# Performance work log

Hardware: AMD Instinct MI355X
Metric: run time of the kernel (lower is better)

## Reference

```python
import jax, jax.numpy as jnp
import numpy as np

B, S, D, A, E = 32, 2048, 512, 64, 64
EPS = 1e-5

def setup_inputs() -> dict:
    key = jax.random.key(0)
    ks = jax.random.split(key, 12)
    sc = 0.02
    return {
        "source_embedding": jax.random.normal(ks[0], (B, E), jnp.float32),
        "inputs": jax.random.normal(ks[1], (B, S, D), jnp.float32),
        "down_w_W": sc * jax.random.normal(ks[2], (E, A * D), jnp.float32),
        "down_w_b": jnp.zeros((A * D,), jnp.float32),
        "down_b_W": sc * jax.random.normal(ks[3], (E, A), jnp.float32),
        "down_b_b": jnp.zeros((A,), jnp.float32),
        "up_w_W": sc * jax.random.normal(ks[4], (E, D * A), jnp.float32),
        "up_w_b": jnp.zeros((D * A,), jnp.float32),
        "up_b_W": sc * jax.random.normal(ks[5], (E, D), jnp.float32),
        "up_b_b": jnp.zeros((D,), jnp.float32),
        "pre_w_W": sc * jax.random.normal(ks[6], (E, D), jnp.float32),
        "pre_w_b": jnp.ones((D,), jnp.float32),
        "pre_b_W": sc * jax.random.normal(ks[7], (E, D), jnp.float32),
        "pre_b_b": jnp.zeros((D,), jnp.float32),
        "post_w_W": sc * jax.random.normal(ks[8], (E, D), jnp.float32),
        "post_w_b": jnp.ones((D,), jnp.float32),
        "post_b_W": sc * jax.random.normal(ks[9], (E, D), jnp.float32),
        "post_b_b": jnp.zeros((D,), jnp.float32),
    }

def _cond_ln(x, w, b):
    # x: [B,S,D]; w,b: [B,D] -> per-sample affine layernorm over last dim
    mean = jnp.mean(x, axis=2, keepdims=True)
    var = jnp.mean((x - mean) ** 2, axis=2, keepdims=True) + EPS
    return (x - mean) / jnp.sqrt(var) * w[:, None, :] + b[:, None, :]

def reference(source_embedding, inputs,
              down_w_W, down_w_b, down_b_W, down_b_b,
              up_w_W, up_w_b, up_b_W, up_b_b,
              pre_w_W, pre_w_b, pre_b_W, pre_b_b,
              post_w_W, post_w_b, post_b_W, post_b_b):
    emb = source_embedding  # [B,E]
    # hypernet-generated per-sample adapter weights
    w_down = (emb @ down_w_W + down_w_b).reshape(B, A, D)  # [B,A,D]
    b_down = emb @ down_b_W + down_b_b                      # [B,A]
    w_up = (emb @ up_w_W + up_w_b).reshape(B, D, A)         # [B,D,A]
    b_up = emb @ up_b_W + up_b_b                            # [B,D]
    # conditional pre layernorm
    pre_w = emb @ pre_w_W + pre_w_b
    pre_b = emb @ pre_b_W + pre_b_b
    z = _cond_ln(inputs, pre_w, pre_b)
    # adapter: down-proj, relu, up-proj (matmul with weight.transpose(1,2))
    down = jnp.einsum('bsd,bad->bsa', z, w_down) + b_down[:, None, :]
    mid = jax.nn.relu(down)
    out = jnp.einsum('bsa,bda->bsd', mid, w_up) + b_up[:, None, :]
    # conditional post layernorm
    post_w = emb @ post_w_W + post_w_b
    post_b = emb @ post_b_W + post_b_b
    out = _cond_ln(out, post_w, post_b)
    return out + inputs
```

## Files before the change

### kernel.cpp

```cpp
#include <hip/hip_runtime.h>

#define NB 32
#define NS 2048
#define ND 512
#define NA 64
#define NE 64

typedef __bf16 bf16x8 __attribute__((ext_vector_type(8)));
typedef float f32x4 __attribute__((ext_vector_type(4)));

__device__ __forceinline__ unsigned short f2bf(float f) {
    union { float f; unsigned u; } v; v.f = f;
    unsigned r = (v.u + 0x7fffu + ((v.u >> 16) & 1u)) >> 16;
    return (unsigned short)r;
}
__device__ __forceinline__ unsigned pk(float a, float b) {
    return (unsigned)f2bf(a) | ((unsigned)f2bf(b) << 16);
}

__global__ __launch_bounds__(256) void hyper_vec(
    const float* __restrict__ emb,
    const float* __restrict__ pwW, const float* __restrict__ pwb,
    const float* __restrict__ pbW, const float* __restrict__ pbb,
    const float* __restrict__ powW, const float* __restrict__ powb,
    const float* __restrict__ pobW, const float* __restrict__ pobb,
    const float* __restrict__ ubW, const float* __restrict__ ubb,
    const float* __restrict__ dbW, const float* __restrict__ dbb,
    float* __restrict__ vecs) {
    int gid = blockIdx.x * 256 + threadIdx.x;
    if (gid >= NB * 2624) return;
    int b = gid / 2624;
    int r = gid - b * 2624;
    const float* W; const float* bias; int off, width;
    if (r < 2560) {
        int v = r >> 9; off = r & 511; width = 512;
        switch (v) {
            case 0:  W = pwW;  bias = pwb;  break;
            case 1:  W = pbW;  bias = pbb;  break;
            case 2:  W = powW; bias = powb; break;
            case 3:  W = pobW; bias = pobb; break;
            default: W = ubW;  bias = ubb;  break;
        }
    } else {
        off = r - 2560; width = 64; W = dbW; bias = dbb;
    }
    float acc = bias[off];
    const float* e = emb + b * 64;
#pragma unroll 8
    for (int k = 0; k < 64; ++k) acc = fmaf(e[k], W[k * width + off], acc);
    vecs[gid] = acc;
}

__global__ __launch_bounds__(256) void hyper_pack(
    const float* __restrict__ emb,
    const float* __restrict__ dwW, const float* __restrict__ dwb,
    const float* __restrict__ uwW, const float* __restrict__ uwb,
    const float* __restrict__ vecs,
    unsigned short* __restrict__ wdfrag, unsigned short* __restrict__ wufrag,
    float* __restrict__ cvec) {
    __shared__ float Wt[64][128];
    __shared__ float embs[NB * NE];
    const int tid = threadIdx.x;
    const int lane = tid & 63;
    const int bx = blockIdx.x;
    const int mat = bx >> 8;
    const int chunk = bx & 255;
    const int base = chunk * 128;
    const int colo = tid & 127;
    const int bh = tid >> 7;
    const float* W = mat ? uwW : dwW;
    const float* bias = mat ? uwb : dwb;

    for (int i = tid; i < NB * NE; i += 256) embs[i] = emb[i];
    for (int i = tid; i < 64 * 32; i += 256) {
        int k = i >> 5, c = (i & 31) << 2;
        *(float4*)&Wt[k][c] = *(const float4*)&W[(size_t)k * 32768 + base + c];
    }
    __syncthreads();

    const int col = base + colo;
    const float bv = bias[col];
    float acc[16];
#pragma unroll
    for (int b = 0; b < 16; ++b) acc[b] = bv;

    for (int k0 = 0; k0 < 64; k0 += 4) {
        float w0 = Wt[k0][colo], w1 = Wt[k0 + 1][colo];
        float w2 = Wt[k0 + 2][colo], w3 = Wt[k0 + 3][colo];
#pragma unroll
        for (int b = 0; b < 16; ++b) {
            float4 e = *(const float4*)&embs[(bh * 16 + b) * 64 + k0];
            acc[b] = fmaf(e.x, w0, acc[b]);
            acc[b] = fmaf(e.y, w1, acc[b]);
            acc[b] = fmaf(e.z, w2, acc[b]);
            acc[b] = fmaf(e.w, w3, acc[b]);
        }
    }

    if (mat == 0) {
        int a = col >> 9, d = col & 511;
        size_t idx0 = ((size_t)((a >> 4) * 16 + (d >> 5)) * 64 +
                       (((d & 31) >> 3) * 16 + (a & 15))) * 8 + (d & 7);
#pragma unroll
        for (int b = 0; b < 16; ++b) {
            int bg = bh * 16 + b;
            float raw = acc[b];
            float pw = vecs[bg * 2624 + d];
            float pb = vecs[bg * 2624 + 512 + d];
            float f = raw * pw;
            wdfrag[idx0 + (size_t)bg * 32768] = f2bf(f);
            float c2v = f, c1v = raw * pb;
#pragma unroll
            for (int m = 1; m <= 32; m <<= 1) {
                c2v += __shfl_xor(c2v, m);
                c1v += __shfl_xor(c1v, m);
            }
            if (lane == 0) {
                atomicAdd(&cvec[bg * 128 + 2 * a], c1v);
                atomicAdd(&cvec[bg * 128 + 2 * a + 1], c2v);
            }
        }
    } else {
        int d = col >> 6, a = col & 63;
        size_t idx0 = ((size_t)((d >> 4) * 2 + (a >> 5)) * 64 +
                       (((a & 31) >> 3) * 16 + (d & 15))) * 8 + (a & 7);
#pragma unroll
        for (int b = 0; b < 16; ++b)
            wufrag[idx0 + (size_t)(bh * 16 + b) * 32768] = f2bf(acc[b]);
    }
}

__global__ __launch_bounds__(256, 5) void fused_adapter(
    const float* __restrict__ inp,
    const unsigned short* __restrict__ wdfold,
    const unsigned short* __restrict__ wufrag,
    const float* __restrict__ vecs,
    const float* __restrict__ cvec,
    float* __restrict__ out) {
    __shared__ __align__(16) unsigned short z_lds[16][520];
    __shared__ __align__(16) unsigned short mid_lds[16][72];
    __shared__ __align__(16) float coeff[1536];
    __shared__ __align__(16) float preS[16][4], preQ[16][4];
    __shared__ __align__(16) float postS[16][4], postQ[16][4];

    const int tid = threadIdx.x;
    const int lane = tid & 63;
    const int wave = tid >> 6;
    const int lanelo = lane & 15;
    const int quad = lane >> 4;
    const int bx = blockIdx.x;
    const int b = bx >> 7;
    const int s0 = (bx & 127) * 16;

    const float* vb = vecs + b * 2624;
    for (int i = tid; i < 384; i += 256)
        ((float4*)coeff)[i] = ((const float4*)(vb + 1024))[i];

    const float* xp = inp + ((size_t)b * NS + s0 + lanelo) * ND + wave * 128 + quad * 8;
    float s = 0.f, q = 0.f;
#pragma unroll
    for (int kc2 = 0; kc2 < 4; ++kc2) {
        float4 x0 = *(const float4*)(xp + kc2 * 32);
        float4 x1 = *(const float4*)(xp + kc2 * 32 + 4);
        s += (x0.x + x0.y + x0.z + x0.w) + (x1.x + x1.y + x1.z + x1.w);
        q = fmaf(x0.x, x0.x, q); q = fmaf(x0.y, x0.y, q);
        q = fmaf(x0.z, x0.z, q); q = fmaf(x0.w, x0.w, q);
        q = fmaf(x1.x, x1.x, q); q = fmaf(x1.y, x1.y, q);
        q = fmaf(x1.z, x1.z, q); q = fmaf(x1.w, x1.w, q);
        uint4 au;
        au.x = pk(x0.x, x0.y); au.y = pk(x0.z, x0.w);
        au.z = pk(x1.x, x1.y); au.w = pk(x1.z, x1.w);
        *(uint4*)&z_lds[lanelo][wave * 128 + kc2 * 32 + quad * 8] = au;
    }
    s += __shfl_xor(s, 16); s += __shfl_xor(s, 32);
    q += __shfl_xor(q, 16); q += __shfl_xor(q, 32);
    if (lane < 16) { preS[lane][wave] = s; preQ[lane][wave] = q; }
    __syncthreads();

    float rs[4], mrs[4];
#pragma unroll
    for (int r = 0; r < 4; ++r) {
        int row = quad * 4 + r;
        float4 S = *(const float4*)preS[row];
        float4 Q = *(const float4*)preQ[row];
        float ss = (S.x + S.y) + (S.z + S.w);
        float qq = (Q.x + Q.y) + (Q.z + Q.w);
        float mean = ss * (1.0f / 512.0f);
        float var = qq * (1.0f / 512.0f) - mean * mean;
        float rstd = rsqrtf(var + 1e-5f);
        rs[r] = rstd;
        mrs[r] = mean * rstd;
    }

    const unsigned short* wd = wdfold + (size_t)b * 32768;
    f32x4 accd = (f32x4){0.f, 0.f, 0.f, 0.f};
#pragma unroll
    for (int kc = 0; kc < 16; ++kc) {
        uint4 au = *(const uint4*)&z_lds[lanelo][kc * 32 + quad * 8];
        uint4 bu = *(const uint4*)(wd + ((size_t)(wave * 16 + kc) * 64 + lane) * 8);
        accd = __builtin_amdgcn_mfma_f32_16x16x32_bf16(
            __builtin_bit_cast(bf16x8, au), __builtin_bit_cast(bf16x8, bu), accd, 0, 0, 0);
    }
    const int a_col = wave * 16 + lanelo;
    float2 cc = *(const float2*)(cvec + b * 128 + 2 * a_col);
    float c1 = cc.x + vb[2560 + a_col];
#pragma unroll
    for (int r = 0; r < 4; ++r) {
        float v = fmaf(rs[r], accd[r], fmaf(-mrs[r], cc.y, c1));
        mid_lds[quad * 4 + r][a_col] = f2bf(fmaxf(v, 0.0f));
    }
    __syncthreads();

    uint4 a0u = *(const uint4*)&mid_lds[lanelo][quad * 8];
    uint4 a1u = *(const uint4*)&mid_lds[lanelo][32 + quad * 8];
    bf16x8 af0 = __builtin_bit_cast(bf16x8, a0u);
    bf16x8 af1 = __builtin_bit_cast(bf16x8, a1u);
    const unsigned short* wu = wufrag + (size_t)b * 32768;
    f32x4 acc8[8];
    float sum[4] = {0.f, 0.f, 0.f, 0.f}, sq[4] = {0.f, 0.f, 0.f, 0.f};
#pragma unroll
    for (int nt8 = 0; nt8 < 8; ++nt8) {
        int nt = wave * 8 + nt8;
        uint4 b0 = *(const uint4*)(wu + ((size_t)(nt * 2 + 0) * 64 + lane) * 8);
        uint4 b1 = *(const uint4*)(wu + ((size_t)(nt * 2 + 1) * 64 + lane) * 8);
        f32x4 a4 = (f32x4){0.f, 0.f, 0.f, 0.f};
        a4 = __builtin_amdgcn_mfma_f32_16x16x32_bf16(af0, __builtin_bit_cast(bf16x8, b0), a4, 0, 0, 0);
        a4 = __builtin_amdgcn_mfma_f32_16x16x32_bf16(af1, __builtin_bit_cast(bf16x8, b1), a4, 0, 0, 0);
        float bu = coeff[1024 + nt * 16 + lanelo];
#pragma unroll
        for (int r = 0; r < 4; ++r) {
            float y = a4[r] + bu;
            a4[r] = y;
            sum[r] += y;
            sq[r] = fmaf(y, y, sq[r]);
        }
        acc8[nt8] = a4;
    }
#pragma unroll
    for (int r = 0; r < 4; ++r) {
#pragma unroll
        for (int m = 1; m <= 8; m <<= 1) {
            sum[r] += __shfl_xor(sum[r], m);
            sq[r] += __shfl_xor(sq[r], m);
        }
    }
    if (lanelo == 0) {
#pragma unroll
        for (int r = 0; r < 4; ++r) {
            postS[quad * 4 + r][wave] = sum[r];
            postQ[quad * 4 + r][wave] = sq[r];
        }
    }
    __syncthreads();

    float mean2[4], rstd2[4];
#pragma unroll
    for (int r = 0; r < 4; ++r) {
        int row = quad * 4 + r;
        float4 S = *(const float4*)postS[row];
        float4 Q = *(const float4*)postQ[row];
        float ss = (S.x + S.y) + (S.z + S.w);
        float qq = (Q.x + Q.y) + (Q.z + Q.w);
        mean2[r] = ss * (1.0f / 512.0f);
        float v2 = qq * (1.0f / 512.0f) - mean2[r] * mean2[r];
        rstd2[r] = rsqrtf(v2 + 1e-5f);
    }

    const size_t obase = ((size_t)b * NS + s0) * ND;
#pragma unroll
    for (int nt8 = 0; nt8 < 8; ++nt8) {
        int col = (wave * 8 + nt8) * 16 + lanelo;
        float pw = coeff[col];
        float pb = coeff[512 + col];
#pragma unroll
        for (int r = 0; r < 4; ++r) {
            size_t off = obase + (size_t)(quad * 4 + r) * ND + col;
            out[off] = fmaf((acc8[nt8][r] - mean2[r]) * rstd2[r], pw, pb) + inp[off];
        }
    }
}

extern "C" void kernel_launch(void* const* d_in, const int* in_sizes, int n_in,
                              void* d_out, int out_size, void* d_ws, size_t ws_size,
                              hipStream_t stream) {
    const float* emb  = (const float*)d_in[0];
    const float* inp  = (const float*)d_in[1];
    const float* dwW  = (const float*)d_in[2];
    const float* dwb  = (const float*)d_in[3];
    const float* dbW  = (const float*)d_in[4];
    const float* dbb  = (const float*)d_in[5];
    const float* uwW  = (const float*)d_in[6];
    const float* uwb  = (const float*)d_in[7];
    const float* ubW  = (const float*)d_in[8];
    const float* ubb  = (const float*)d_in[9];
    const float* pwW  = (const float*)d_in[10];
    const float* pwb  = (const float*)d_in[11];
    const float* pbW  = (const float*)d_in[12];
    const float* pbb  = (const float*)d_in[13];
    const float* powW = (const float*)d_in[14];
    const float* powb = (const float*)d_in[15];
    const float* pobW = (const float*)d_in[16];
    const float* pobb = (const float*)d_in[17];

    unsigned short* wdfrag = (unsigned short*)d_ws;
    unsigned short* wufrag = wdfrag + (size_t)NB * 32768;
    float* vecs = (float*)(wufrag + (size_t)NB * 32768);
    float* cvec = vecs + (size_t)NB * 2624;

    hyper_vec<<<(NB * 2624 + 255) / 256, 256, 0, stream>>>(
        emb, pwW, pwb, pbW, pbb, powW, powb, pobW, pobb, ubW, ubb, dbW, dbb, vecs);
    hipMemsetAsync(cvec, 0, (size_t)NB * 128 * sizeof(float), stream);
    hyper_pack<<<512, 256, 0, stream>>>(emb, dwW, dwb, uwW, uwb, vecs,
                                        wdfrag, wufrag, cvec);
    fused_adapter<<<NB * (NS / 16), 256, 0, stream>>>(
        inp, wdfrag, wufrag, vecs, cvec, (float*)d_out);
}
```

Baseline: 331.9 us.

## Split down-projection over K across waves with LDS partial-sum reduction

```diff
diff --git a/kernel.cpp b/kernel.cpp
--- a/kernel.cpp
+++ b/kernel.cpp
@@ -130,14 +130,14 @@
     }
 }
 
-__global__ __launch_bounds__(256, 5) void fused_adapter(
+__global__ __launch_bounds__(256, 4) void fused_adapter(
     const float* __restrict__ inp,
     const unsigned short* __restrict__ wdfold,
     const unsigned short* __restrict__ wufrag,
     const float* __restrict__ vecs,
     const float* __restrict__ cvec,
     float* __restrict__ out) {
-    __shared__ __align__(16) unsigned short z_lds[16][520];
+    __shared__ __align__(16) float p_lds[4][16][68];
     __shared__ __align__(16) unsigned short mid_lds[16][72];
     __shared__ __align__(16) float coeff[1536];
     __shared__ __align__(16) float preS[16][4], preQ[16][4];
@@ -148,39 +148,66 @@
     const int wave = tid >> 6;
     const int lanelo = lane & 15;
     const int quad = lane >> 4;
-    const int bx = blockIdx.x;
+    const int bx0 = blockIdx.x;
+    const int bx = (bx0 & 7) * 512 + (bx0 >> 3);
     const int b = bx >> 7;
     const int s0 = (bx & 127) * 16;
 
     const float* vb = vecs + b * 2624;
+
+    const float* xp = inp + ((size_t)b * NS + s0 + lanelo) * ND + wave * 128 + quad * 8;
+    float4 x0[4], x1[4];
+#pragma unroll
+    for (int kc2 = 0; kc2 < 4; ++kc2) {
+        x0[kc2] = *(const float4*)(xp + kc2 * 32);
+        x1[kc2] = *(const float4*)(xp + kc2 * 32 + 4);
+    }
+
     for (int i = tid; i < 384; i += 256)
         ((float4*)coeff)[i] = ((const float4*)(vb + 1024))[i];
 
-    const float* xp = inp + ((size_t)b * NS + s0 + lanelo) * ND + wave * 128 + quad * 8;
+    uint4 au[4];
     float s = 0.f, q = 0.f;
 #pragma unroll
     for (int kc2 = 0; kc2 < 4; ++kc2) {
-        float4 x0 = *(const float4*)(xp + kc2 * 32);
-        float4 x1 = *(const float4*)(xp + kc2 * 32 + 4);
-        s += (x0.x + x0.y + x0.z + x0.w) + (x1.x + x1.y + x1.z + x1.w);
-        q = fmaf(x0.x, x0.x, q); q = fmaf(x0.y, x0.y, q);
-        q = fmaf(x0.z, x0.z, q); q = fmaf(x0.w, x0.w, q);
-        q = fmaf(x1.x, x1.x, q); q = fmaf(x1.y, x1.y, q);
-        q = fmaf(x1.z, x1.z, q); q = fmaf(x1.w, x1.w, q);
-        uint4 au;
-        au.x = pk(x0.x, x0.y); au.y = pk(x0.z, x0.w);
-        au.z = pk(x1.x, x1.y); au.w = pk(x1.z, x1.w);
-        *(uint4*)&z_lds[lanelo][wave * 128 + kc2 * 32 + quad * 8] = au;
+        float4 a = x0[kc2], c = x1[kc2];
+        s += (a.x + a.y + a.z + a.w) + (c.x + c.y + c.z + c.w);
+        q = fmaf(a.x, a.x, q); q = fmaf(a.y, a.y, q);
+        q = fmaf(a.z, a.z, q); q = fmaf(a.w, a.w, q);
+        q = fmaf(c.x, c.x, q); q = fmaf(c.y, c.y, q);
+        q = fmaf(c.z, c.z, q); q = fmaf(c.w, c.w, q);
+        au[kc2].x = pk(a.x, a.y); au[kc2].y = pk(a.z, a.w);
+        au[kc2].z = pk(c.x, c.y); au[kc2].w = pk(c.z, c.w);
     }
     s += __shfl_xor(s, 16); s += __shfl_xor(s, 32);
     q += __shfl_xor(q, 16); q += __shfl_xor(q, 32);
     if (lane < 16) { preS[lane][wave] = s; preQ[lane][wave] = q; }
+
+    const unsigned short* wd = wdfold + (size_t)b * 32768;
+    const unsigned short* wdp = wd + ((size_t)(wave * 4) * 64 + lane) * 8;
+    f32x4 acc[4];
+#pragma unroll
+    for (int nt = 0; nt < 4; ++nt) acc[nt] = (f32x4){0.f, 0.f, 0.f, 0.f};
+#pragma unroll
+    for (int kc2 = 0; kc2 < 4; ++kc2) {
+        bf16x8 af = __builtin_bit_cast(bf16x8, au[kc2]);
+#pragma unroll
+        for (int nt = 0; nt < 4; ++nt) {
+            uint4 bu = *(const uint4*)(wdp + (size_t)(nt * 16 + kc2) * 512);
+            acc[nt] = __builtin_amdgcn_mfma_f32_16x16x32_bf16(
+                af, __builtin_bit_cast(bf16x8, bu), acc[nt], 0, 0, 0);
+        }
+    }
+#pragma unroll
+    for (int nt = 0; nt < 4; ++nt)
+#pragma unroll
+        for (int r = 0; r < 4; ++r)
+            p_lds[wave][quad * 4 + r][nt * 16 + lanelo] = acc[nt][r];
     __syncthreads();
 
-    float rs[4], mrs[4];
-#pragma unroll
-    for (int r = 0; r < 4; ++r) {
-        int row = quad * 4 + r;
+    {
+        const int row = tid >> 4;
+        const int a0 = (tid & 15) << 2;
         float4 S = *(const float4*)preS[row];
         float4 Q = *(const float4*)preQ[row];
         float ss = (S.x + S.y) + (S.z + S.w);
@@ -188,26 +215,20 @@
         float mean = ss * (1.0f / 512.0f);
         float var = qq * (1.0f / 512.0f) - mean * mean;
         float rstd = rsqrtf(var + 1e-5f);
-        rs[r] = rstd;
-        mrs[r] = mean * rstd;
-    }
-
-    const unsigned short* wd = wdfold + (size_t)b * 32768;
-    f32x4 accd = (f32x4){0.f, 0.f, 0.f, 0.f};
-#pragma unroll
-    for (int kc = 0; kc < 16; ++kc) {
-        uint4 au = *(const uint4*)&z_lds[lanelo][kc * 32 + quad * 8];
-        uint4 bu = *(const uint4*)(wd + ((size_t)(wave * 16 + kc) * 64 + lane) * 8);
-        accd = __builtin_amdgcn_mfma_f32_16x16x32_bf16(
-            __builtin_bit_cast(bf16x8, au), __builtin_bit_cast(bf16x8, bu), accd, 0, 0, 0);
-    }
-    const int a_col = wave * 16 + lanelo;
-    float2 cc = *(const float2*)(cvec + b * 128 + 2 * a_col);
-    float c1 = cc.x + vb[2560 + a_col];
-#pragma unroll
-    for (int r = 0; r < 4; ++r) {
-        float v = fmaf(rs[r], accd[r], fmaf(-mrs[r], cc.y, c1));
-        mid_lds[quad * 4 + r][a_col] = f2bf(fmaxf(v, 0.0f));
+        float mrs = mean * rstd;
+        f32x4 v = *(const f32x4*)&p_lds[0][row][a0];
+        v = v + *(const f32x4*)&p_lds[1][row][a0];
+        v = v + *(const f32x4*)&p_lds[2][row][a0];
+        v = v + *(const f32x4*)&p_lds[3][row][a0];
+        float4 cv0 = *(const float4*)&cvec[b * 128 + 2 * a0];
+        float4 cv1 = *(const float4*)&cvec[b * 128 + 2 * a0 + 4];
+        float4 bd = *(const float4*)&vb[2560 + a0];
+        ushort4 m;
+        m.x = f2bf(fmaxf(fmaf(rstd, v[0], fmaf(-mrs, cv0.y, cv0.x + bd.x)), 0.f));
+        m.y = f2bf(fmaxf(fmaf(rstd, v[1], fmaf(-mrs, cv0.w, cv0.z + bd.y)), 0.f));
+        m.z = f2bf(fmaxf(fmaf(rstd, v[2], fmaf(-mrs, cv1.y, cv1.x + bd.z)), 0.f));
+        m.w = f2bf(fmaxf(fmaf(rstd, v[3], fmaf(-mrs, cv1.w, cv1.z + bd.w)), 0.f));
+        *(ushort4*)&mid_lds[row][a0] = m;
     }
     __syncthreads();
 
```

Measured after the change: 338.5 us. +2.0%, slower.

## Process four 16-row tiles per block with register prefetch of next tile

Applied to the files above, without the earlier changes.

```diff
diff --git a/kernel.cpp b/kernel.cpp
--- a/kernel.cpp
+++ b/kernel.cpp
@@ -130,7 +130,7 @@
     }
 }
 
-__global__ __launch_bounds__(256, 5) void fused_adapter(
+__global__ __launch_bounds__(256, 4) void fused_adapter(
     const float* __restrict__ inp,
     const unsigned short* __restrict__ wdfold,
     const unsigned short* __restrict__ wufrag,
@@ -148,134 +148,156 @@
     const int wave = tid >> 6;
     const int lanelo = lane & 15;
     const int quad = lane >> 4;
-    const int bx = blockIdx.x;
-    const int b = bx >> 7;
-    const int s0 = (bx & 127) * 16;
+    const int bx0 = blockIdx.x;
+    const int bx = (bx0 & 7) * 128 + (bx0 >> 3);
+    const int b = bx >> 5;
+    const int s_base = (bx & 31) * 64;
+
+    const float* xpw = inp + ((size_t)b * NS + s_base + lanelo) * ND + wave * 128 + quad * 8;
+    float4 x0[4], x1[4];
+#pragma unroll
+    for (int kc2 = 0; kc2 < 4; ++kc2) {
+        x0[kc2] = *(const float4*)(xpw + kc2 * 32);
+        x1[kc2] = *(const float4*)(xpw + kc2 * 32 + 4);
+    }
 
     const float* vb = vecs + b * 2624;
     for (int i = tid; i < 384; i += 256)
         ((float4*)coeff)[i] = ((const float4*)(vb + 1024))[i];
 
-    const float* xp = inp + ((size_t)b * NS + s0 + lanelo) * ND + wave * 128 + quad * 8;
-    float s = 0.f, q = 0.f;
-#pragma unroll
-    for (int kc2 = 0; kc2 < 4; ++kc2) {
-        float4 x0 = *(const float4*)(xp + kc2 * 32);
-        float4 x1 = *(const float4*)(xp + kc2 * 32 + 4);
-        s += (x0.x + x0.y + x0.z + x0.w) + (x1.x + x1.y + x1.z + x1.w);
-        q = fmaf(x0.x, x0.x, q); q = fmaf(x0.y, x0.y, q);
-        q = fmaf(x0.z, x0.z, q); q = fmaf(x0.w, x0.w, q);
-        q = fmaf(x1.x, x1.x, q); q = fmaf(x1.y, x1.y, q);
-        q = fmaf(x1.z, x1.z, q); q = fmaf(x1.w, x1.w, q);
-        uint4 au;
-        au.x = pk(x0.x, x0.y); au.y = pk(x0.z, x0.w);
-        au.z = pk(x1.x, x1.y); au.w = pk(x1.z, x1.w);
-        *(uint4*)&z_lds[lanelo][wave * 128 + kc2 * 32 + quad * 8] = au;
-    }
-    s += __shfl_xor(s, 16); s += __shfl_xor(s, 32);
-    q += __shfl_xor(q, 16); q += __shfl_xor(q, 32);
-    if (lane < 16) { preS[lane][wave] = s; preQ[lane][wave] = q; }
-    __syncthreads();
-
-    float rs[4], mrs[4];
-#pragma unroll
-    for (int r = 0; r < 4; ++r) {
-        int row = quad * 4 + r;
-        float4 S = *(const float4*)preS[row];
-        float4 Q = *(const float4*)preQ[row];
-        float ss = (S.x + S.y) + (S.z + S.w);
-        float qq = (Q.x + Q.y) + (Q.z + Q.w);
-        float mean = ss * (1.0f / 512.0f);
-        float var = qq * (1.0f / 512.0f) - mean * mean;
-        float rstd = rsqrtf(var + 1e-5f);
-        rs[r] = rstd;
-        mrs[r] = mean * rstd;
-    }
-
     const unsigned short* wd = wdfold + (size_t)b * 32768;
-    f32x4 accd = (f32x4){0.f, 0.f, 0.f, 0.f};
-#pragma unroll
-    for (int kc = 0; kc < 16; ++kc) {
-        uint4 au = *(const uint4*)&z_lds[lanelo][kc * 32 + quad * 8];
-        uint4 bu = *(const uint4*)(wd + ((size_t)(wave * 16 + kc) * 64 + lane) * 8);
-        accd = __builtin_amdgcn_mfma_f32_16x16x32_bf16(
-            __builtin_bit_cast(bf16x8, au), __builtin_bit_cast(bf16x8, bu), accd, 0, 0, 0);
-    }
+    const unsigned short* wu = wufrag + (size_t)b * 32768;
     const int a_col = wave * 16 + lanelo;
-    float2 cc = *(const float2*)(cvec + b * 128 + 2 * a_col);
-    float c1 = cc.x + vb[2560 + a_col];
-#pragma unroll
-    for (int r = 0; r < 4; ++r) {
-        float v = fmaf(rs[r], accd[r], fmaf(-mrs[r], cc.y, c1));
-        mid_lds[quad * 4 + r][a_col] = f2bf(fmaxf(v, 0.0f));
-    }
-    __syncthreads();
-
-    uint4 a0u = *(const uint4*)&mid_lds[lanelo][quad * 8];
-    uint4 a1u = *(const uint4*)&mid_lds[lanelo][32 + quad * 8];
-    bf16x8 af0 = __builtin_bit_cast(bf16x8, a0u);
-    bf16x8 af1 = __builtin_bit_cast(bf16x8, a1u);
-    const unsigned short* wu = wufrag + (size_t)b * 32768;
-    f32x4 acc8[8];
-    float sum[4] = {0.f, 0.f, 0.f, 0.f}, sq[4] = {0.f, 0.f, 0.f, 0.f};
-#pragma unroll
-    for (int nt8 = 0; nt8 < 8; ++nt8) {
-        int nt = wave * 8 + nt8;
-        uint4 b0 = *(const uint4*)(wu + ((size_t)(nt * 2 + 0) * 64 + lane) * 8);
-        uint4 b1 = *(const uint4*)(wu + ((size_t)(nt * 2 + 1) * 64 + lane) * 8);
-        f32x4 a4 = (f32x4){0.f, 0.f, 0.f, 0.f};
-        a4 = __builtin_amdgcn_mfma_f32_16x16x32_bf16(af0, __builtin_bit_cast(bf16x8, b0), a4, 0, 0, 0);
-        a4 = __builtin_amdgcn_mfma_f32_16x16x32_bf16(af1, __builtin_bit_cast(bf16x8, b1), a4, 0, 0, 0);
-        float bu = coeff[1024 + nt * 16 + lanelo];
+    const float2 cc = *(const float2*)(cvec + b * 128 + 2 * a_col);
+    const float c1 = cc.x + vb[2560 + a_col];
+
+    for (int t = 0; t < 4; ++t) {
+        float s = 0.f, q = 0.f;
+#pragma unroll
+        for (int kc2 = 0; kc2 < 4; ++kc2) {
+            float4 a = x0[kc2], c = x1[kc2];
+            s += (a.x + a.y + a.z + a.w) + (c.x + c.y + c.z + c.w);
+            q = fmaf(a.x, a.x, q); q = fmaf(a.y, a.y, q);
+            q = fmaf(a.z, a.z, q); q = fmaf(a.w, a.w, q);
+            q = fmaf(c.x, c.x, q); q = fmaf(c.y, c.y, q);
+            q = fmaf(c.z, c.z, q); q = fmaf(c.w, c.w, q);
+            uint4 au;
+            au.x = pk(a.x, a.y); au.y = pk(a.z, a.w);
+            au.z = pk(c.x, c.y); au.w = pk(c.z, c.w);
+            *(uint4*)&z_lds[lanelo][wave * 128 + kc2 * 32 + quad * 8] = au;
+        }
+        s += __shfl_xor(s, 16); s += __shfl_xor(s, 32);
+        q += __shfl_xor(q, 16); q += __shfl_xor(q, 32);
+        if (lane < 16) { preS[lane][wave] = s; preQ[lane][wave] = q; }
+
+        if (t < 3) {
+            const float* xn = xpw + (size_t)(t + 1) * 16 * ND;
+#pragma unroll
+            for (int kc2 = 0; kc2 < 4; ++kc2) {
+                x0[kc2] = *(const float4*)(xn + kc2 * 32);
+                x1[kc2] = *(const float4*)(xn + kc2 * 32 + 4);
+            }
+        }
+        asm volatile("s_waitcnt lgkmcnt(0)" ::: "memory");
+        __builtin_amdgcn_s_barrier();
+
+        float rs[4], mrs[4];
 #pragma unroll
         for (int r = 0; r < 4; ++r) {
-            float y = a4[r] + bu;
-            a4[r] = y;
-            sum[r] += y;
-            sq[r] = fmaf(y, y, sq[r]);
-        }
-        acc8[nt8] = a4;
-    }
-#pragma unroll
-    for (int r = 0; r < 4; ++r) {
-#pragma unroll
-        for (int m = 1; m <= 8; m <<= 1) {
-            sum[r] += __shfl_xor(sum[r], m);
-            sq[r] += __shfl_xor(sq[r], m);
-        }
-    }
-    if (lanelo == 0) {
+            int row = quad * 4 + r;
+            float4 S = *(const float4*)preS[row];
+            float4 Q = *(const float4*)preQ[row];
+            float ss = (S.x + S.y) + (S.z + S.w);
+            float qq = (Q.x + Q.y) + (Q.z + Q.w);
+            float mean = ss * (1.0f / 512.0f);
+            float var = qq * (1.0f / 512.0f) - mean * mean;
+            float rstd = rsqrtf(var + 1e-5f);
+            rs[r] = rstd;
+            mrs[r] = mean * rstd;
+        }
+
+        f32x4 accd = (f32x4){0.f, 0.f, 0.f, 0.f};
+#pragma unroll
+        for (int kc = 0; kc < 16; ++kc) {
+            uint4 azu = *(const uint4*)&z_lds[lanelo][kc * 32 + quad * 8];
+            uint4 bu = *(const uint4*)(wd + ((size_t)(wave * 16 + kc) * 64 + lane) * 8);
+            accd = __builtin_amdgcn_mfma_f32_16x16x32_bf16(
+                __builtin_bit_cast(bf16x8, azu), __builtin_bit_cast(bf16x8, bu), accd, 0, 0, 0);
+        }
 #pragma unroll
         for (int r = 0; r < 4; ++r) {
-            postS[quad * 4 + r][wave] = sum[r];
-            postQ[quad * 4 + r][wave] = sq[r];
-        }
-    }
-    __syncthreads();
-
-    float mean2[4], rstd2[4];
-#pragma unroll
-    for (int r = 0; r < 4; ++r) {
-        int row = quad * 4 + r;
-        float4 S = *(const float4*)postS[row];
-        float4 Q = *(const float4*)postQ[row];
-        float ss = (S.x + S.y) + (S.z + S.w);
-        float qq = (Q.x + Q.y) + (Q.z + Q.w);
-        mean2[r] = ss * (1.0f / 512.0f);
-        float v2 = qq * (1.0f / 512.0f) - mean2[r] * mean2[r];
-        rstd2[r] = rsqrtf(v2 + 1e-5f);
-    }
-
-    const size_t obase = ((size_t)b * NS + s0) * ND;
-#pragma unroll
-    for (int nt8 = 0; nt8 < 8; ++nt8) {
-        int col = (wave * 8 + nt8) * 16 + lanelo;
-        float pw = coeff[col];
-        float pb = coeff[512 + col];
+            float v = fmaf(rs[r], accd[r], fmaf(-mrs[r], cc.y, c1));
+            mid_lds[quad * 4 + r][a_col] = f2bf(fmaxf(v, 0.0f));
+        }
+        asm volatile("s_waitcnt lgkmcnt(0)" ::: "memory");
+        __builtin_amdgcn_s_barrier();
+
+        uint4 a0u = *(const uint4*)&mid_lds[lanelo][quad * 8];
+        uint4 a1u = *(const uint4*)&mid_lds[lanelo][32 + quad * 8];
+        bf16x8 af0 = __builtin_bit_cast(bf16x8, a0u);
+        bf16x8 af1 = __builtin_bit_cast(bf16x8, a1u);
+        f32x4 acc8[8];
+        float sum[4] = {0.f, 0.f, 0.f, 0.f}, sq[4] = {0.f, 0.f, 0.f, 0.f};
+#pragma unroll
+        for (int nt8 = 0; nt8 < 8; ++nt8) {
+            int nt = wave * 8 + nt8;
+            uint4 b0 = *(const uint4*)(wu + ((size_t)(nt * 2 + 0) * 64 + lane) * 8);
+            uint4 b1 = *(const uint4*)(wu + ((size_t)(nt * 2 + 1) * 64 + lane) * 8);
+            f32x4 a4 = (f32x4){0.f, 0.f, 0.f, 0.f};
+            a4 = __builtin_amdgcn_mfma_f32_16x16x32_bf16(af0, __builtin_bit_cast(bf16x8, b0), a4, 0, 0, 0);
+            a4 = __builtin_amdgcn_mfma_f32_16x16x32_bf16(af1, __builtin_bit_cast(bf16x8, b1), a4, 0, 0, 0);
+            float bu = coeff[1024 + nt * 16 + lanelo];
+#pragma unroll
+            for (int r = 0; r < 4; ++r) {
+                float y = a4[r] + bu;
+                a4[r] = y;
+                sum[r] += y;
+                sq[r] = fmaf(y, y, sq[r]);
+            }
+            acc8[nt8] = a4;
+        }
 #pragma unroll
         for (int r = 0; r < 4; ++r) {
-            size_t off = obase + (size_t)(quad * 4 + r) * ND + col;
-            out[off] = fmaf((acc8[nt8][r] - mean2[r]) * rstd2[r], pw, pb) + inp[off];
+#pragma unroll
+            for (int m = 1; m <= 8; m <<= 1) {
+                sum[r] += __shfl_xor(sum[r], m);
+                sq[r] += __shfl_xor(sq[r], m);
+            }
+        }
+        if (lanelo == 0) {
+#pragma unroll
+            for (int r = 0; r < 4; ++r) {
+                postS[quad * 4 + r][wave] = sum[r];
+                postQ[quad * 4 + r][wave] = sq[r];
+            }
+        }
+        asm volatile("s_waitcnt lgkmcnt(0)" ::: "memory");
+        __builtin_amdgcn_s_barrier();
+
+        float mean2[4], rstd2[4];
+#pragma unroll
+        for (int r = 0; r < 4; ++r) {
+            int row = quad * 4 + r;
+            float4 S = *(const float4*)postS[row];
+            float4 Q = *(const float4*)postQ[row];
+            float ss = (S.x + S.y) + (S.z + S.w);
+            float qq = (Q.x + Q.y) + (Q.z + Q.w);
+            mean2[r] = ss * (1.0f / 512.0f);
+            float v2 = qq * (1.0f / 512.0f) - mean2[r] * mean2[r];
+            rstd2[r] = rsqrtf(v2 + 1e-5f);
+        }
+
+        const size_t obase = ((size_t)b * NS + s_base + t * 16) * ND;
+#pragma unroll
+        for (int nt8 = 0; nt8 < 8; ++nt8) {
+            int col = (wave * 8 + nt8) * 16 + lanelo;
+            float pw = coeff[col];
+            float pb = coeff[512 + col];
+#pragma unroll
+            for (int r = 0; r < 4; ++r) {
+                size_t off = obase + (size_t)(quad * 4 + r) * ND + col;
+                out[off] = fmaf((acc8[nt8][r] - mean2[r]) * rstd2[r], pw, pb) + inp[off];
+            }
         }
     }
 }
@@ -312,6 +334,6 @@
     hipMemsetAsync(cvec, 0, (size_t)NB * 128 * sizeof(float), stream);
     hyper_pack<<<512, 256, 0, stream>>>(emb, dwW, dwb, uwW, uwb, vecs,
                                         wdfrag, wufrag, cvec);
-    fused_adapter<<<NB * (NS / 16), 256, 0, stream>>>(
+    fused_adapter<<<NB * (NS / 64), 256, 0, stream>>>(
         inp, wdfrag, wufrag, vecs, cvec, (float*)d_out);
 }
```

Measured after the change: 423.2 us. 27.5% more time.

## Prefetch adapter weight fragments, swizzle block order, use lightweight LDS barriers

Applied to the files above, without the earlier changes.

```diff
diff --git a/kernel.cpp b/kernel.cpp
--- a/kernel.cpp
+++ b/kernel.cpp
@@ -17,6 +17,9 @@
 __device__ __forceinline__ unsigned pk(float a, float b) {
     return (unsigned)f2bf(a) | ((unsigned)f2bf(b) << 16);
 }
+
+#define BAR() do { asm volatile("s_waitcnt lgkmcnt(0)" ::: "memory"); \
+                   __builtin_amdgcn_s_barrier(); } while (0)
 
 __global__ __launch_bounds__(256) void hyper_vec(
     const float* __restrict__ emb,
@@ -130,7 +133,7 @@
     }
 }
 
-__global__ __launch_bounds__(256, 5) void fused_adapter(
+__global__ __launch_bounds__(256, 4) void fused_adapter(
     const float* __restrict__ inp,
     const unsigned short* __restrict__ wdfold,
     const unsigned short* __restrict__ wufrag,
@@ -148,7 +151,8 @@
     const int wave = tid >> 6;
     const int lanelo = lane & 15;
     const int quad = lane >> 4;
-    const int bx = blockIdx.x;
+    const int bx0 = blockIdx.x;
+    const int bx = (bx0 & 7) * 512 + (bx0 >> 3);
     const int b = bx >> 7;
     const int s0 = (bx & 127) * 16;
 
@@ -175,7 +179,21 @@
     s += __shfl_xor(s, 16); s += __shfl_xor(s, 32);
     q += __shfl_xor(q, 16); q += __shfl_xor(q, 32);
     if (lane < 16) { preS[lane][wave] = s; preQ[lane][wave] = q; }
-    __syncthreads();
+
+    const unsigned short* wd = wdfold + (size_t)b * 32768;
+    const unsigned short* wu = wufrag + (size_t)b * 32768;
+    uint4 bw[4];
+#pragma unroll
+    for (int i = 0; i < 4; ++i)
+        bw[i] = *(const uint4*)(wd + ((size_t)(wave * 16 + i) * 64 + lane) * 8);
+    uint4 bb[2][2];
+#pragma unroll
+    for (int i = 0; i < 2; ++i) {
+        int nt = wave * 8 + i;
+        bb[i][0] = *(const uint4*)(wu + ((size_t)(nt * 2 + 0) * 64 + lane) * 8);
+        bb[i][1] = *(const uint4*)(wu + ((size_t)(nt * 2 + 1) * 64 + lane) * 8);
+    }
+    BAR();
 
     float rs[4], mrs[4];
 #pragma unroll
@@ -192,14 +210,15 @@
         mrs[r] = mean * rstd;
     }
 
-    const unsigned short* wd = wdfold + (size_t)b * 32768;
     f32x4 accd = (f32x4){0.f, 0.f, 0.f, 0.f};
 #pragma unroll
     for (int kc = 0; kc < 16; ++kc) {
-        uint4 au = *(const uint4*)&z_lds[lanelo][kc * 32 + quad * 8];
-        uint4 bu = *(const uint4*)(wd + ((size_t)(wave * 16 + kc) * 64 + lane) * 8);
+        uint4 azu = *(const uint4*)&z_lds[lanelo][kc * 32 + quad * 8];
+        uint4 bu = bw[kc & 3];
+        if (kc < 12)
+            bw[kc & 3] = *(const uint4*)(wd + ((size_t)(wave * 16 + kc + 4) * 64 + lane) * 8);
         accd = __builtin_amdgcn_mfma_f32_16x16x32_bf16(
-            __builtin_bit_cast(bf16x8, au), __builtin_bit_cast(bf16x8, bu), accd, 0, 0, 0);
+            __builtin_bit_cast(bf16x8, azu), __builtin_bit_cast(bf16x8, bu), accd, 0, 0, 0);
     }
     const int a_col = wave * 16 + lanelo;
     float2 cc = *(const float2*)(cvec + b * 128 + 2 * a_col);
@@ -209,20 +228,23 @@
         float v = fmaf(rs[r], accd[r], fmaf(-mrs[r], cc.y, c1));
         mid_lds[quad * 4 + r][a_col] = f2bf(fmaxf(v, 0.0f));
     }
-    __syncthreads();
+    BAR();
 
     uint4 a0u = *(const uint4*)&mid_lds[lanelo][quad * 8];
     uint4 a1u = *(const uint4*)&mid_lds[lanelo][32 + quad * 8];
     bf16x8 af0 = __builtin_bit_cast(bf16x8, a0u);
     bf16x8 af1 = __builtin_bit_cast(bf16x8, a1u);
-    const unsigned short* wu = wufrag + (size_t)b * 32768;
     f32x4 acc8[8];
     float sum[4] = {0.f, 0.f, 0.f, 0.f}, sq[4] = {0.f, 0.f, 0.f, 0.f};
 #pragma unroll
     for (int nt8 = 0; nt8 < 8; ++nt8) {
         int nt = wave * 8 + nt8;
-        uint4 b0 = *(const uint4*)(wu + ((size_t)(nt * 2 + 0) * 64 + lane) * 8);
-        uint4 b1 = *(const uint4*)(wu + ((size_t)(nt * 2 + 1) * 64 + lane) * 8);
+        uint4 b0 = bb[nt8 & 1][0];
+        uint4 b1 = bb[nt8 & 1][1];
+        if (nt8 < 6) {
+            bb[nt8 & 1][0] = *(const uint4*)(wu + ((size_t)((nt + 2) * 2 + 0) * 64 + lane) * 8);
+            bb[nt8 & 1][1] = *(const uint4*)(wu + ((size_t)((nt + 2) * 2 + 1) * 64 + lane) * 8);
+        }
         f32x4 a4 = (f32x4){0.f, 0.f, 0.f, 0.f};
         a4 = __builtin_amdgcn_mfma_f32_16x16x32_bf16(af0, __builtin_bit_cast(bf16x8, b0), a4, 0, 0, 0);
         a4 = __builtin_amdgcn_mfma_f32_16x16x32_bf16(af1, __builtin_bit_cast(bf16x8, b1), a4, 0, 0, 0);
@@ -251,7 +273,7 @@
             postQ[quad * 4 + r][wave] = sq[r];
         }
     }
-    __syncthreads();
+    BAR();
 
     float mean2[4], rstd2[4];
 #pragma unroll
```

New measurement: 340.1 us. +2.5%, slower.
